# Kernel optimization log

Hardware: AMD Instinct MI355X
Metric: run time of the kernel (lower is better)

## Reference

```python
import jax, jax.numpy as jnp
import numpy as np

MASK_W = 1.0
KPT_W = 0.5

SOBEL_X = jnp.array([[-1.0, 0.0, 1.0], [-2.0, 0.0, 2.0], [-1.0, 0.0, 1.0]], jnp.float32).reshape(1, 1, 3, 3)
SOBEL_Y = jnp.array([[-1.0, -2.0, -1.0], [0.0, 0.0, 0.0], [1.0, 2.0, 1.0]], jnp.float32).reshape(1, 1, 3, 3)
BOX = jnp.ones((1, 1, 3, 3), jnp.float32)


def conv3x3(x, k):
    # x: [N,1,H,W]; torch F.conv2d is cross-correlation, same as lax conv
    return jax.lax.conv_general_dilated(
        x, k, window_strides=(1, 1), padding=[(1, 1), (1, 1)],
        dimension_numbers=('NCHW', 'OIHW', 'NCHW'))


def sobel_edge(mask):
    ex = conv3x3(mask, SOBEL_X)
    ey = conv3x3(mask, SOBEL_Y)
    return jnp.sqrt(ex * ex + ey * ey)


def grid_sample_bilinear_zeros(img, grid):
    # img: [H,W]; grid: [K,2] in [-1,1], (x,y) order; align_corners=False, zero padding
    H, W = img.shape
    x = (grid[:, 0] + 1.0) * (W * 0.5) - 0.5
    y = (grid[:, 1] + 1.0) * (H * 0.5) - 0.5
    x0 = jnp.floor(x).astype(jnp.int32)
    y0 = jnp.floor(y).astype(jnp.int32)
    x1 = x0 + 1
    y1 = y0 + 1
    wx1 = x - x0.astype(x.dtype)
    wx0 = 1.0 - wx1
    wy1 = y - y0.astype(y.dtype)
    wy0 = 1.0 - wy1

    def gather(ix, iy):
        valid = (ix >= 0) & (ix < W) & (iy >= 0) & (iy < H)
        v = img[jnp.clip(iy, 0, H - 1), jnp.clip(ix, 0, W - 1)]
        return jnp.where(valid, v, 0.0)

    return (wx0 * wy0 * gather(x0, y0) + wx1 * wy0 * gather(x1, y0)
            + wx0 * wy1 * gather(x0, y1) + wx1 * wy1 * gather(x1, y1))


def setup_inputs() -> dict:
    key = jax.random.key(0)
    k1, k2, k3, k4 = jax.random.split(key, 4)
    return {
        'pred_keypoints': jax.random.uniform(k1, (1024, 2), jnp.float32),
        'target_keypoints': jax.random.uniform(k2, (1024, 2), jnp.float32),
        'pred_seg': jax.random.uniform(k3, (1, 1, 4096, 4096), jnp.float32),
        'target_seg': jax.random.uniform(k4, (1, 1, 4096, 4096), jnp.float32),
    }


def reference(pred_keypoints, target_keypoints, pred_seg, target_seg):
    target_edge = sobel_edge(target_seg)
    pred_edge = sobel_edge(pred_seg)
    edge_loss = jnp.mean((pred_edge - target_edge) ** 2)
    distance_map = conv3x3(pred_edge, BOX)  # [1,1,H,W]
    kd = grid_sample_bilinear_zeros(distance_map[0, 0], pred_keypoints)  # [K]
    constraint_loss = jnp.mean(kd)
    return MASK_W * edge_loss + KPT_W * constraint_loss
```

## Files before the change

### kernel.cpp

```cpp
#include <hip/hip_runtime.h>

#define H 4096
#define W 4096
#define TH 16
#define BX 256
#define GX 4
#define GY (H / TH)
#define NEDGE (GX * GY)
#define NKPB 16

#define MASK_W 1.0f
#define KPT_W 0.5f

struct RowData { float v0, v1, v2, v3, lf, rf; };
struct Prep { float dx0, dx1, dx2, dx3, s0, s1, s2, s3; };

__device__ __forceinline__ float fast_sqrt(float x) {
    return __builtin_amdgcn_sqrtf(x);
}

__device__ __forceinline__ RowData loadrow_fast(const float* __restrict__ rowptr,
                                                int c, bool rvalid) {
    float4 v;
    if (rvalid) v = *(const float4*)rowptr;
    else        v = make_float4(0.f, 0.f, 0.f, 0.f);
    RowData rd;
    rd.v0 = v.x; rd.v1 = v.y; rd.v2 = v.z; rd.v3 = v.w;
    rd.lf = __shfl_up(v.w, 1);
    rd.rf = __shfl_down(v.x, 1);
    int lane = threadIdx.x & 63;
    if (lane == 0 || lane == 63) {
        bool left = (lane == 0);
        bool ok = rvalid && (left ? (c > 0) : (c + 4 < W));
        const float* q = left ? (rowptr - 1) : (rowptr + 4);
        float h = ok ? *q : 0.f;
        if (left) rd.lf = h; else rd.rf = h;
    }
    return rd;
}

__device__ __forceinline__ Prep prep(const RowData& rd) {
    Prep o;
    o.dx0 = rd.v1 - rd.lf;
    o.dx1 = rd.v2 - rd.v0;
    o.dx2 = rd.v3 - rd.v1;
    o.dx3 = rd.rf - rd.v2;
    o.s0 = __fmaf_rn(2.f, rd.v0, rd.lf + rd.v1);
    o.s1 = __fmaf_rn(2.f, rd.v1, rd.v0 + rd.v2);
    o.s2 = __fmaf_rn(2.f, rd.v2, rd.v1 + rd.v3);
    o.s3 = __fmaf_rn(2.f, rd.v3, rd.v2 + rd.rf);
    return o;
}

__device__ __forceinline__ float edge1(float dxA, float dxB, float dxC, float sA, float sC) {
    float ex = dxA + __fmaf_rn(2.f, dxB, dxC);
    float ey = sC - sA;
    return fast_sqrt(__fmaf_rn(ex, ex, ey * ey));
}

__global__ __launch_bounds__(BX) void fused_kernel(const float* __restrict__ pred,
                                                   const float* __restrict__ targ,
                                                   const float* __restrict__ kp,
                                                   float* __restrict__ ws) {
    int bid = blockIdx.x;

    if (bid < NEDGE) {
        int gx = bid & (GX - 1);
        int gy = bid >> 2;
        int c  = gx * (BX * 4) + threadIdx.x * 4;
        int r0 = gy * TH;

        const float* prow = pred + (size_t)r0 * W + c;
        const float* trow = targ + (size_t)r0 * W + c;

        Prep pA = prep(loadrow_fast(prow - W, c, r0 > 0));
        Prep pB = prep(loadrow_fast(prow,     c, true));
        Prep tA = prep(loadrow_fast(trow - W, c, r0 > 0));
        Prep tB = prep(loadrow_fast(trow,     c, true));
        RowData pn = loadrow_fast(prow + W, c, true);
        RowData tn = loadrow_fast(trow + W, c, true);
        prow += 2 * (size_t)W;
        trow += 2 * (size_t)W;

        float acc = 0.f;
        #pragma unroll 4
        for (int i = 0; i < TH; ++i) {
            RowData pc = pn, tc = tn;
            if (i < TH - 1) {
                bool nvalid = (r0 + i + 2) < H;
                pn = loadrow_fast(prow, c, nvalid);
                tn = loadrow_fast(trow, c, nvalid);
                prow += W; trow += W;
            }
            Prep pC = prep(pc);
            Prep tC = prep(tc);

            float pe, te, d;
            pe = edge1(pA.dx0, pB.dx0, pC.dx0, pA.s0, pC.s0);
            te = edge1(tA.dx0, tB.dx0, tC.dx0, tA.s0, tC.s0);
            d = pe - te; acc = __fmaf_rn(d, d, acc);
            pe = edge1(pA.dx1, pB.dx1, pC.dx1, pA.s1, pC.s1);
            te = edge1(tA.dx1, tB.dx1, tC.dx1, tA.s1, tC.s1);
            d = pe - te; acc = __fmaf_rn(d, d, acc);
            pe = edge1(pA.dx2, pB.dx2, pC.dx2, pA.s2, pC.s2);
            te = edge1(tA.dx2, tB.dx2, tC.dx2, tA.s2, tC.s2);
            d = pe - te; acc = __fmaf_rn(d, d, acc);
            pe = edge1(pA.dx3, pB.dx3, pC.dx3, pA.s3, pC.s3);
            te = edge1(tA.dx3, tB.dx3, tC.dx3, tA.s3, tC.s3);
            d = pe - te; acc = __fmaf_rn(d, d, acc);

            pA = pB; pB = pC;
            tA = tB; tB = tC;
        }

        #pragma unroll
        for (int m = 32; m; m >>= 1) acc += __shfl_xor(acc, m);

        __shared__ float wsum[BX / 64];
        if ((threadIdx.x & 63) == 0) wsum[threadIdx.x >> 6] = acc;
        __syncthreads();
        if (threadIdx.x == 0) {
            float s = 0.f;
            #pragma unroll
            for (int i = 0; i < BX / 64; ++i) s += wsum[i];
            ws[bid] = s;
        }
    } else {
        int t = threadIdx.x;
        if (t >= 64) return;
        int k = (bid - NEDGE) * 64 + t;

        float gx = kp[2 * k];
        float gy = kp[2 * k + 1];
        float x = (gx + 1.f) * (W * 0.5f) - 0.5f;
        float y = (gy + 1.f) * (H * 0.5f) - 0.5f;
        float fx0 = floorf(x), fy0 = floorf(y);
        int x0 = (int)fx0, y0 = (int)fy0;
        int x1 = x0 + 1, y1 = y0 + 1;
        float wx1 = x - fx0, wx0 = 1.f - wx1;
        float wy1 = y - fy0, wy0 = 1.f - wy1;

        float sg[6][6];
        #pragma unroll
        for (int i = 0; i < 6; ++i) {
            int rr = y0 - 2 + i;
            #pragma unroll
            for (int j = 0; j < 6; ++j) {
                int cc = x0 - 2 + j;
                bool ok = (rr >= 0) & (rr < H) & (cc >= 0) & (cc < W);
                sg[i][j] = ok ? pred[(size_t)rr * W + cc] : 0.f;
            }
        }

        float e[4][4];
        #pragma unroll
        for (int i = 0; i < 4; ++i) {
            int rr = y0 - 1 + i;
            #pragma unroll
            for (int j = 0; j < 4; ++j) {
                int cc = x0 - 1 + j;
                if (rr < 0 || rr >= H || cc < 0 || cc >= W) { e[i][j] = 0.f; continue; }
                float ex = (sg[i][j + 2] - sg[i][j])
                         + 2.f * (sg[i + 1][j + 2] - sg[i + 1][j])
                         + (sg[i + 2][j + 2] - sg[i + 2][j]);
                float ey = (sg[i + 2][j] + 2.f * sg[i + 2][j + 1] + sg[i + 2][j + 2])
                         - (sg[i][j] + 2.f * sg[i][j + 1] + sg[i][j + 2]);
                e[i][j] = fast_sqrt(__fmaf_rn(ex, ex, ey * ey));
            }
        }

        float dmap[2][2];
        #pragma unroll
        for (int a = 0; a < 2; ++a) {
            #pragma unroll
            for (int b = 0; b < 2; ++b) {
                float s = 0.f;
                #pragma unroll
                for (int i = 0; i < 3; ++i)
                    #pragma unroll
                    for (int j = 0; j < 3; ++j) s += e[a + i][b + j];
                dmap[a][b] = s;
            }
        }

        bool vx0 = (x0 >= 0) & (x0 < W), vx1 = (x1 >= 0) & (x1 < W);
        bool vy0 = (y0 >= 0) & (y0 < H), vy1 = (y1 >= 0) & (y1 < H);
        float v00 = (vx0 & vy0) ? dmap[0][0] : 0.f;
        float v01 = (vx1 & vy0) ? dmap[0][1] : 0.f;
        float v10 = (vx0 & vy1) ? dmap[1][0] : 0.f;
        float v11 = (vx1 & vy1) ? dmap[1][1] : 0.f;
        float kd = wx0 * wy0 * v00 + wx1 * wy0 * v01
                 + wx0 * wy1 * v10 + wx1 * wy1 * v11;

        #pragma unroll
        for (int m = 32; m; m >>= 1) kd += __shfl_xor(kd, m);
        if (t == 0) ws[NEDGE + (bid - NEDGE)] = kd;
    }
}

__global__ __launch_bounds__(256) void final_kernel(const float* __restrict__ ws,
                                                    float* __restrict__ out) {
    int t = threadIdx.x;
    float es = 0.f;
    #pragma unroll
    for (int i = 0; i < NEDGE / 256; ++i) es += ws[t + i * 256];
    float ks = (t < NKPB) ? ws[NEDGE + t] : 0.f;

    #pragma unroll
    for (int m = 32; m; m >>= 1) {
        es += __shfl_xor(es, m);
        ks += __shfl_xor(ks, m);
    }
    __shared__ float res[4], rks[4];
    int wid = t >> 6;
    if ((t & 63) == 0) { res[wid] = es; rks[wid] = ks; }
    __syncthreads();
    if (t == 0) {
        float e2 = res[0] + res[1] + res[2] + res[3];
        float k2 = rks[0] + rks[1] + rks[2] + rks[3];
        float edge_loss = e2 * (1.f / ((float)H * (float)W));
        float constraint_loss = k2 * (1.f / 1024.f);
        out[0] = MASK_W * edge_loss + KPT_W * constraint_loss;
    }
}

extern "C" void kernel_launch(void* const* d_in, const int* in_sizes, int n_in,
                              void* d_out, int out_size, void* d_ws, size_t ws_size,
                              hipStream_t stream) {
    const float* kp   = (const float*)d_in[0];
    const float* pred = (const float*)d_in[2];
    const float* targ = (const float*)d_in[3];
    float* out = (float*)d_out;
    float* ws  = (float*)d_ws;

    fused_kernel<<<NEDGE + NKPB, BX, 0, stream>>>(pred, targ, kp, ws);
    final_kernel<<<1, 256, 0, stream>>>(ws, out);
}
```

Before: 168.9 us.

## Split row loads from lane shuffles and halve rows per block

Separates the global loads (including the halo loads for edge lanes) from the cross-lane shuffles. This lets the loads for the next row be issued before the shuffles of the current row, so memory latency is not serialized behind shuffle waits. It also halves the rows per block from 16 to 8, doubling the block count, and fully unrolls the row loop. In exchange the redundant halo row reads grow from 2/16 to 2/8 per tile, and register pressure rises from holding raw rows across iterations.

After: 155.7 us. 1.08x faster.

```diff
diff --git a/kernel.cpp b/kernel.cpp
--- a/kernel.cpp
+++ b/kernel.cpp
@@ -2,7 +2,7 @@
 
 #define H 4096
 #define W 4096
-#define TH 16
+#define TH 8
 #define BX 256
 #define GX 4
 #define GY (H / TH)
@@ -12,6 +12,7 @@
 #define MASK_W 1.0f
 #define KPT_W 0.5f
 
+struct Raw { float4 v; float lf, rf; };
 struct RowData { float v0, v1, v2, v3, lf, rf; };
 struct Prep { float dx0, dx1, dx2, dx3, s0, s1, s2, s3; };
 
@@ -19,23 +20,24 @@
     return __builtin_amdgcn_sqrtf(x);
 }
 
-__device__ __forceinline__ RowData loadrow_fast(const float* __restrict__ rowptr,
-                                                int c, bool rvalid) {
-    float4 v;
-    if (rvalid) v = *(const float4*)rowptr;
-    else        v = make_float4(0.f, 0.f, 0.f, 0.f);
+__device__ __forceinline__ Raw loadraw(const float* __restrict__ rowptr,
+                                       int c, bool rvalid, int lane) {
+    Raw r;
+    if (rvalid) r.v = *(const float4*)rowptr;
+    else        r.v = make_float4(0.f, 0.f, 0.f, 0.f);
+    r.lf = 0.f; r.rf = 0.f;
+    if (lane == 0)  { if (rvalid & (c > 0))     r.lf = rowptr[-1]; }
+    if (lane == 63) { if (rvalid & (c + 4 < W)) r.rf = rowptr[4];  }
+    return r;
+}
+
+__device__ __forceinline__ RowData finalize(const Raw& r, int lane) {
     RowData rd;
-    rd.v0 = v.x; rd.v1 = v.y; rd.v2 = v.z; rd.v3 = v.w;
-    rd.lf = __shfl_up(v.w, 1);
-    rd.rf = __shfl_down(v.x, 1);
-    int lane = threadIdx.x & 63;
-    if (lane == 0 || lane == 63) {
-        bool left = (lane == 0);
-        bool ok = rvalid && (left ? (c > 0) : (c + 4 < W));
-        const float* q = left ? (rowptr - 1) : (rowptr + 4);
-        float h = ok ? *q : 0.f;
-        if (left) rd.lf = h; else rd.rf = h;
-    }
+    rd.v0 = r.v.x; rd.v1 = r.v.y; rd.v2 = r.v.z; rd.v3 = r.v.w;
+    float lf = __shfl_up(r.v.w, 1);
+    float rf = __shfl_down(r.v.x, 1);
+    rd.lf = (lane == 0)  ? r.lf : lf;
+    rd.rf = (lane == 63) ? r.rf : rf;
     return rd;
 }
 
@@ -69,31 +71,37 @@
         int gy = bid >> 2;
         int c  = gx * (BX * 4) + threadIdx.x * 4;
         int r0 = gy * TH;
+        int lane = threadIdx.x & 63;
 
         const float* prow = pred + (size_t)r0 * W + c;
         const float* trow = targ + (size_t)r0 * W + c;
 
-        Prep pA = prep(loadrow_fast(prow - W, c, r0 > 0));
-        Prep pB = prep(loadrow_fast(prow,     c, true));
-        Prep tA = prep(loadrow_fast(trow - W, c, r0 > 0));
-        Prep tB = prep(loadrow_fast(trow,     c, true));
-        RowData pn = loadrow_fast(prow + W, c, true);
-        RowData tn = loadrow_fast(trow + W, c, true);
+        Raw rpA = loadraw(prow - W, c, r0 > 0, lane);
+        Raw rtA = loadraw(trow - W, c, r0 > 0, lane);
+        Raw rpB = loadraw(prow,     c, true,   lane);
+        Raw rtB = loadraw(trow,     c, true,   lane);
+        Raw rpn = loadraw(prow + W, c, true,   lane);
+        Raw rtn = loadraw(trow + W, c, true,   lane);
         prow += 2 * (size_t)W;
         trow += 2 * (size_t)W;
 
+        Prep pA = prep(finalize(rpA, lane));
+        Prep tA = prep(finalize(rtA, lane));
+        Prep pB = prep(finalize(rpB, lane));
+        Prep tB = prep(finalize(rtB, lane));
+
         float acc = 0.f;
-        #pragma unroll 4
+        #pragma unroll
         for (int i = 0; i < TH; ++i) {
-            RowData pc = pn, tc = tn;
+            Raw rpc = rpn, rtc = rtn;
             if (i < TH - 1) {
-                bool nvalid = (r0 + i + 2) < H;
-                pn = loadrow_fast(prow, c, nvalid);
-                tn = loadrow_fast(trow, c, nvalid);
+                bool nv = (r0 + i + 2) < H;
+                rpn = loadraw(prow, c, nv, lane);
+                rtn = loadraw(trow, c, nv, lane);
                 prow += W; trow += W;
             }
-            Prep pC = prep(pc);
-            Prep tC = prep(tc);
+            Prep pC = prep(finalize(rpc, lane));
+            Prep tC = prep(finalize(rtc, lane));
 
             float pe, te, d;
             pe = edge1(pA.dx0, pB.dx0, pC.dx0, pA.s0, pC.s0);
```

## Shrink row tile to 4 and preload all halo rows up front

Applied to the files above, without the earlier changes.

Each edge block now covers 4 rows instead of 16, so the grid has four times as many blocks. Every thread issues all six float4 row loads (plus edge-lane halo scalars) for pred and target before it computes anything, and the compute loop is fully unrolled. The aim is to keep more memory requests in flight and raise occupancy, replacing the serial one-row-ahead software pipeline. In exchange, the two halo rows are re-read for every 4 output rows, which adds redundant traffic that L2 may or may not absorb, and register use per thread goes up.

Measured after the change: 154.6 us. 1.09x faster.

```diff
diff --git a/kernel.cpp b/kernel.cpp
--- a/kernel.cpp
+++ b/kernel.cpp
@@ -2,7 +2,8 @@
 
 #define H 4096
 #define W 4096
-#define TH 16
+#define TH 4
+#define NR (TH + 2)
 #define BX 256
 #define GX 4
 #define GY (H / TH)
@@ -12,43 +13,26 @@
 #define MASK_W 1.0f
 #define KPT_W 0.5f
 
-struct RowData { float v0, v1, v2, v3, lf, rf; };
 struct Prep { float dx0, dx1, dx2, dx3, s0, s1, s2, s3; };
 
 __device__ __forceinline__ float fast_sqrt(float x) {
     return __builtin_amdgcn_sqrtf(x);
 }
 
-__device__ __forceinline__ RowData loadrow_fast(const float* __restrict__ rowptr,
-                                                int c, bool rvalid) {
-    float4 v;
-    if (rvalid) v = *(const float4*)rowptr;
-    else        v = make_float4(0.f, 0.f, 0.f, 0.f);
-    RowData rd;
-    rd.v0 = v.x; rd.v1 = v.y; rd.v2 = v.z; rd.v3 = v.w;
-    rd.lf = __shfl_up(v.w, 1);
-    rd.rf = __shfl_down(v.x, 1);
-    int lane = threadIdx.x & 63;
-    if (lane == 0 || lane == 63) {
-        bool left = (lane == 0);
-        bool ok = rvalid && (left ? (c > 0) : (c + 4 < W));
-        const float* q = left ? (rowptr - 1) : (rowptr + 4);
-        float h = ok ? *q : 0.f;
-        if (left) rd.lf = h; else rd.rf = h;
-    }
-    return rd;
-}
-
-__device__ __forceinline__ Prep prep(const RowData& rd) {
+__device__ __forceinline__ Prep fin(float4 v, float h, bool isL, bool isR) {
+    float lf = __shfl_up(v.w, 1);
+    float rf = __shfl_down(v.x, 1);
+    lf = isL ? h : lf;
+    rf = isR ? h : rf;
     Prep o;
-    o.dx0 = rd.v1 - rd.lf;
-    o.dx1 = rd.v2 - rd.v0;
-    o.dx2 = rd.v3 - rd.v1;
-    o.dx3 = rd.rf - rd.v2;
-    o.s0 = __fmaf_rn(2.f, rd.v0, rd.lf + rd.v1);
-    o.s1 = __fmaf_rn(2.f, rd.v1, rd.v0 + rd.v2);
-    o.s2 = __fmaf_rn(2.f, rd.v2, rd.v1 + rd.v3);
-    o.s3 = __fmaf_rn(2.f, rd.v3, rd.v2 + rd.rf);
+    o.dx0 = v.y - lf;
+    o.dx1 = v.z - v.x;
+    o.dx2 = v.w - v.y;
+    o.dx3 = rf  - v.z;
+    o.s0 = __fmaf_rn(2.f, v.x, lf  + v.y);
+    o.s1 = __fmaf_rn(2.f, v.y, v.x + v.z);
+    o.s2 = __fmaf_rn(2.f, v.z, v.y + v.w);
+    o.s3 = __fmaf_rn(2.f, v.w, v.z + rf);
     return o;
 }
 
@@ -69,31 +53,42 @@
         int gy = bid >> 2;
         int c  = gx * (BX * 4) + threadIdx.x * 4;
         int r0 = gy * TH;
-
-        const float* prow = pred + (size_t)r0 * W + c;
-        const float* trow = targ + (size_t)r0 * W + c;
-
-        Prep pA = prep(loadrow_fast(prow - W, c, r0 > 0));
-        Prep pB = prep(loadrow_fast(prow,     c, true));
-        Prep tA = prep(loadrow_fast(trow - W, c, r0 > 0));
-        Prep tB = prep(loadrow_fast(trow,     c, true));
-        RowData pn = loadrow_fast(prow + W, c, true);
-        RowData tn = loadrow_fast(trow + W, c, true);
-        prow += 2 * (size_t)W;
-        trow += 2 * (size_t)W;
+        int lane = threadIdx.x & 63;
+        bool isL = (lane == 0), isR = (lane == 63);
+        bool haloCol = (isL & (c > 0)) | (isR & (c + 4 < W));
+
+        const float* bp = pred + (size_t)r0 * W + c;
+        const float* bt = targ + (size_t)r0 * W + c;
+
+        float4 pv[NR], tv[NR];
+        float  hp[NR], ht[NR];
+        #pragma unroll
+        for (int r = 0; r < NR; ++r) {
+            int row = r0 - 1 + r;
+            bool valid = (unsigned)row < (unsigned)H;
+            const float* pp = bp + (ptrdiff_t)(r - 1) * W;
+            const float* tt = bt + (ptrdiff_t)(r - 1) * W;
+            pv[r] = valid ? *(const float4*)pp : make_float4(0.f, 0.f, 0.f, 0.f);
+            tv[r] = valid ? *(const float4*)tt : make_float4(0.f, 0.f, 0.f, 0.f);
+            float h1 = 0.f, h2 = 0.f;
+            if (valid & haloCol) {
+                const float* q1 = isL ? pp - 1 : pp + 4;
+                const float* q2 = isL ? tt - 1 : tt + 4;
+                h1 = *q1; h2 = *q2;
+            }
+            hp[r] = h1; ht[r] = h2;
+        }
+
+        Prep pA = fin(pv[0], hp[0], isL, isR);
+        Prep tA = fin(tv[0], ht[0], isL, isR);
+        Prep pB = fin(pv[1], hp[1], isL, isR);
+        Prep tB = fin(tv[1], ht[1], isL, isR);
 
         float acc = 0.f;
-        #pragma unroll 4
+        #pragma unroll
         for (int i = 0; i < TH; ++i) {
-            RowData pc = pn, tc = tn;
-            if (i < TH - 1) {
-                bool nvalid = (r0 + i + 2) < H;
-                pn = loadrow_fast(prow, c, nvalid);
-                tn = loadrow_fast(trow, c, nvalid);
-                prow += W; trow += W;
-            }
-            Prep pC = prep(pc);
-            Prep tC = prep(tc);
+            Prep pC = fin(pv[i + 2], hp[i + 2], isL, isR);
+            Prep tC = fin(tv[i + 2], ht[i + 2], isL, isR);
 
             float pe, te, d;
             pe = edge1(pA.dx0, pB.dx0, pC.dx0, pA.s0, pC.s0);
```
